# Kernel tuning notes

Hardware: AMD Instinct MI355X
Metric: run time of the kernel (lower is better)

The kernel has to match this reference:

```python
import jax, jax.numpy as jnp
import numpy as np


def setup_inputs() -> dict:
    key = jax.random.key(0)
    k = jax.random.split(key, 6)
    BS, T, ZCH, H, W = 16, 8, 256, 16, 16
    VOCAB, EMB = 4096, 256
    x = jax.random.uniform(k[0], (BS, T, ZCH, H, W), dtype=jnp.float32)
    # Embedding init mirrors uniform_(-1/vocab, 1/vocab)
    codebook = jax.random.uniform(k[1], (VOCAB, EMB), dtype=jnp.float32,
                                  minval=-1.0 / VOCAB, maxval=1.0 / VOCAB)
    pre_w = jax.random.normal(k[2], (EMB, ZCH), dtype=jnp.float32) * 0.02
    pre_b = jax.random.normal(k[3], (EMB,), dtype=jnp.float32) * 0.02
    post_w = jax.random.normal(k[4], (ZCH, EMB), dtype=jnp.float32) * 0.02
    post_b = jax.random.normal(k[5], (ZCH,), dtype=jnp.float32) * 0.02
    return {"x": x, "codebook": codebook, "pre_w": pre_w, "pre_b": pre_b,
            "post_w": post_w, "post_b": post_b}


def reference(x, codebook, pre_w, pre_b, post_w, post_b):
    bs, t, zch, h, w = x.shape
    vocab, emb = codebook.shape
    # preprocess: [0,1] -> [-1,1]
    xp = x * 2.0 - 1.0
    # flatten time into batch; encoder is identity (external module)
    z_in = xp.reshape(bs * t, zch, h, w)
    # pre_quantize_conv: 1x1 conv == per-pixel linear (z_ch -> emb)
    z = jnp.einsum('bchw,ec->behw', z_in, pre_w) + pre_b[None, :, None, None]
    # flatten: (b h w) e  -- matches rearrange('b e h w -> (b h w) e')
    zf = z.transpose(0, 2, 3, 1).reshape(-1, emb)  # [N, emb]
    # squared cdist via expansion: ||z||^2 + ||c||^2 - 2 z.c
    z_sq = jnp.sum(zf * zf, axis=-1, keepdims=True)          # [N,1]
    c_sq = jnp.sum(codebook * codebook, axis=-1)             # [V]
    dist = z_sq + c_sq[None, :] - 2.0 * (zf @ codebook.T)    # [N,V]
    tokens = jnp.argmin(dist, axis=-1)                        # [N]
    zq = codebook[tokens]                                     # [N, emb] gather
    zq = zq.reshape(bs * t, h, w, emb).transpose(0, 3, 1, 2)  # b e h w
    # straight-through estimator
    dec_in = z + jax.lax.stop_gradient(zq - z)
    # post_quantize_conv: 1x1 conv (emb -> z_ch); decoder is identity
    recon = jnp.einsum('behw,ce->bchw', dec_in, post_w) + post_b[None, :, None, None]
    z_out = z.reshape(bs, t, emb, h, w)
    zq_out = zq.reshape(bs, t, emb, h, w)
    recon_out = recon.reshape(bs, t, zch, h, w)
    tokens_out = tokens.reshape(bs, t, h * w)
    return z_out, zq_out, recon_out, tokens_out
```

## Files before the change

kernel.cpp:

```cpp
#include <hip/hip_runtime.h>
#include <float.h>
#include <stdint.h>

#define BB   128
#define CCH  256
#define EMB_ 256
#define HW   256
#define NPIX 32768
#define VOC  4096

typedef _Float16 f16x8 __attribute__((ext_vector_type(8)));
typedef float    f32x4 __attribute__((ext_vector_type(4)));

__device__ __forceinline__ void async16(void* lds, const void* g) {
    __builtin_amdgcn_global_load_lds((const __attribute__((address_space(1))) uint32_t*)g,
                                     (__attribute__((address_space(3))) uint32_t*)lds,
                                     16, 0, 0);
}

__global__ __launch_bounds__(256) void k_prep(const float* __restrict__ cb,
                                              const float* __restrict__ post_w,
                                              const float* __restrict__ post_b,
                                              const float* __restrict__ pre_w,
                                              float* __restrict__ postcode,
                                              _Float16* __restrict__ B3,
                                              float* __restrict__ csq,
                                              _Float16* __restrict__ W3) {
    __shared__ float smem[4352];
    const int bid = blockIdx.x;
    const int tid = threadIdx.x;

    if (bid < 256) {
        float (*cbs)[EMB_] = (float(*)[EMB_])smem;
        int v0 = bid * 16;
        int c  = tid;
#pragma unroll
        for (int r = 0; r < 16; ++r)
            cbs[r][c] = cb[(v0 + r) * EMB_ + c];
        __syncthreads();
        float acc[16];
        float bias = post_b[c];
#pragma unroll
        for (int r = 0; r < 16; ++r) acc[r] = bias;
        const float4* w4p = (const float4*)(post_w + c * EMB_);
        for (int e4 = 0; e4 < 64; ++e4) {
            float4 w4 = w4p[e4];
#pragma unroll
            for (int r = 0; r < 16; ++r) {
                float4 c4 = *(const float4*)&cbs[r][e4 * 4];
                acc[r] = fmaf(w4.x, c4.x, fmaf(w4.y, c4.y,
                         fmaf(w4.z, c4.z, fmaf(w4.w, c4.w, acc[r]))));
            }
        }
#pragma unroll
        for (int r = 0; r < 16; ++r)
            postcode[(v0 + r) * CCH + c] = acc[r];
    } else if (bid < 512) {
        float (*cs)[17] = (float(*)[17])smem;
        int vg = bid - 256;
        int vr = tid >> 4, e0 = (tid & 15) << 4;
        const float* cp = cb + (vg * 16 + vr) * EMB_ + e0;
#pragma unroll
        for (int j = 0; j < 16; ++j)
            cs[e0 + j][vr] = cp[j];
        __syncthreads();
#pragma unroll
        for (int it = 0; it < 4; ++it) {
            int c = it * 256 + tid;
            int kc8 = c >> 4, row = c & 15;
            int lo = kc8 >> 5;
            int kh = kc8 & 31;
            f16x8 outv;
#pragma unroll
            for (int j = 0; j < 8; ++j) {
                float v = cs[kh * 8 + j][row] * 65536.0f;
                _Float16 h = (_Float16)v;
                if (lo) h = (_Float16)(v - (float)h);
                outv[j] = h;
            }
            *(f16x8*)(B3 + ((vg * 64 + kc8) * 128 + row * 8)) = outv;
        }
    } else if (bid < 528) {
        int v = (bid - 512) * 256 + tid;
        const float4* row = (const float4*)(cb + v * EMB_);
        float s = 0.f;
#pragma unroll 8
        for (int q = 0; q < 64; ++q) {
            float4 a = row[q];
            s = fmaf(a.x, a.x, fmaf(a.y, a.y, fmaf(a.z, a.z, fmaf(a.w, a.w, s))));
        }
        csq[v] = s;
    } else {
        int eg = bid - 528;
#pragma unroll
        for (int i = 0; i < 4; ++i) {
            int flat = i * 256 + tid;
            int u = flat >> 4, row = flat & 15;
            int part = u >> 5, c8 = u & 31;
            const float* wp = pre_w + (eg * 16 + row) * CCH + c8 * 8;
            f16x8 outv;
#pragma unroll
            for (int j = 0; j < 8; ++j) {
                float v = wp[j] * 16.0f;
                _Float16 h = (_Float16)v;
                if (part) h = (_Float16)((v - (float)h) * 4096.0f);
                outv[j] = h;
            }
            *(f16x8*)(W3 + ((eg * 64 + u) * 128 + row * 8)) = outv;
        }
    }
}

__global__ __launch_bounds__(512) void k_zgemm(const float* __restrict__ x,
                                               const _Float16* __restrict__ W3,
                                               const float* __restrict__ pre_b,
                                               float* __restrict__ zout,
                                               _Float16* __restrict__ A3) {
    __shared__ __align__(16) char smem[99328];
    float* pbs = (float*)(smem + 98304);

    const int tid = threadIdx.x;
    const int l   = tid & 63;
    const int w   = tid >> 6;
    const int l15 = l & 15, l4 = l >> 4;
    const int wr  = w >> 2, wc = w & 3;
    const int bM  = blockIdx.x;
    const int b   = bM >> 1, hw0 = (bM & 1) * 128;

    const int xng = tid >> 6, xu = (tid >> 4) & 3, xrow = tid & 15;
    const float* xbase = x + (size_t)b * (CCH * HW) + hw0 + xng * 16 + xrow;

#define STAGE_W(CC, BUF) {                                                   \
    _Pragma("unroll")                                                        \
    for (int i = 0; i < 2; ++i) {                                            \
        int flat = i * 512 + tid; int eg = flat >> 6, sub = flat & 63;       \
        async16((_Float16*)(smem + (BUF) * 16384) + flat * 8,                \
                W3 + (eg * 64 + (CC) * 4) * 128 + sub * 8);                  \
        async16((_Float16*)(smem + 32768 + (BUF) * 16384) + flat * 8,        \
                W3 + (eg * 64 + 32 + (CC) * 4) * 128 + sub * 8);             \
    } }

#define STAGE_X(CC, BUF) {                                                   \
    const float* xp_ = xbase + ((CC) * 32 + xu * 8) * HW;                    \
    f16x8 hv, lv;                                                            \
    _Pragma("unroll")                                                        \
    for (int j = 0; j < 8; ++j) {                                            \
        float xv = 2.0f * xp_[j * HW] - 1.0f;                     \
        _Float16 h = (_Float16)xv;                                           \
        lv[j] = (_Float16)((xv - (float)h) * 4096.0f);   \
        hv[j] = h;                                                           \
    }                                                                        \
    *(f16x8*)((_Float16*)(smem + 65536 + (BUF) * 8192) + tid * 8) = hv;      \
    *(f16x8*)((_Float16*)(smem + 81920 + (BUF) * 8192) + tid * 8) = lv;      \
    }

    if (tid < 256) pbs[tid] = pre_b[tid];
    STAGE_W(0, 0)
    STAGE_X(0, 0)
    __syncthreads();

    f32x4 accA[4][4], accB[4][4];
    const f32x4 zero4 = {0.f, 0.f, 0.f, 0.f};
#pragma unroll
    for (int m = 0; m < 4; ++m)
#pragma unroll
        for (int s = 0; s < 4; ++s) { accA[m][s] = zero4; accB[m][s] = zero4; }

    int buf = 0;
    for (int cc = 0; cc < 8; ++cc) {
        if (cc < 7) { STAGE_W(cc + 1, buf ^ 1) STAGE_X(cc + 1, buf ^ 1) }
        const _Float16* WhC = (const _Float16*)(smem + buf * 16384);
        const _Float16* WlC = (const _Float16*)(smem + 32768 + buf * 16384);
        const _Float16* XhC = (const _Float16*)(smem + 65536 + buf * 8192);
        const _Float16* XlC = (const _Float16*)(smem + 81920 + buf * 8192);
        f16x8 whf[4], wlf[4], xhf[4], xlf[4];
#pragma unroll
        for (int m = 0; m < 4; ++m) {
            whf[m] = *(const f16x8*)&WhC[((wc * 4 + m) * 64 + l4 * 16 + l15) * 8];
            wlf[m] = *(const f16x8*)&WlC[((wc * 4 + m) * 64 + l4 * 16 + l15) * 8];
        }
#pragma unroll
        for (int s = 0; s < 4; ++s) {
            xhf[s] = *(const f16x8*)&XhC[((wr * 4 + s) * 64 + l4 * 16 + l15) * 8];
            xlf[s] = *(const f16x8*)&XlC[((wr * 4 + s) * 64 + l4 * 16 + l15) * 8];
        }
#pragma unroll
        for (int m = 0; m < 4; ++m)
#pragma unroll
            for (int s = 0; s < 4; ++s)
                accA[m][s] = __builtin_amdgcn_mfma_f32_16x16x32_f16(whf[m], xhf[s], accA[m][s], 0, 0, 0);
#pragma unroll
        for (int m = 0; m < 4; ++m)
#pragma unroll
            for (int s = 0; s < 4; ++s)
                accB[m][s] = __builtin_amdgcn_mfma_f32_16x16x32_f16(whf[m], xlf[s], accB[m][s], 0, 0, 0);
#pragma unroll
        for (int m = 0; m < 4; ++m)
#pragma unroll
            for (int s = 0; s < 4; ++s)
                accB[m][s] = __builtin_amdgcn_mfma_f32_16x16x32_f16(wlf[m], xhf[s], accB[m][s], 0, 0, 0);
        __syncthreads();
        buf ^= 1;
    }

    float* zw = (float*)(smem + w * 5120);
    const size_t zbase = (size_t)b * (EMB_ * HW) + hw0;
#pragma unroll
    for (int m = 0; m < 4; ++m) {
        asm volatile("s_waitcnt lgkmcnt(0)" ::: "memory");
        __builtin_amdgcn_sched_barrier(0);
        f32x4 zv[4];
#pragma unroll
        for (int s = 0; s < 4; ++s) {
#pragma unroll
            for (int r = 0; r < 4; ++r) {
                float g = fmaf(accB[m][s][r], 0x1p-12f, accA[m][s][r]) * 0x1p-4f;
                zv[s][r] = g + pbs[wc * 64 + m * 16 + l4 * 4 + r];
            }
            *(f32x4*)(zw + (s * 16 + l15) * 20 + l4 * 4) = zv[s];
#pragma unroll
            for (int r = 0; r < 4; ++r)
                zout[zbase + (size_t)(wc * 64 + m * 16 + l4 * 4 + r) * HW
                     + wr * 64 + s * 16 + l15] = zv[s][r];
        }
        asm volatile("s_waitcnt lgkmcnt(0)" ::: "memory");
        __builtin_amdgcn_sched_barrier(0);
#pragma unroll
        for (int o = 0; o < 4; ++o) {
            int flat = o * 64 + l;
            int part = flat >> 7, rest = flat & 127;
            int pg = rest >> 5, uq = (rest >> 4) & 1, row = rest & 15;
            int nloc = pg * 16 + row;
            float4 va = *(const float4*)(zw + nloc * 20 + uq * 8);
            float4 vb = *(const float4*)(zw + nloc * 20 + uq * 8 + 4);
            float vs[8] = {va.x, va.y, va.z, va.w, vb.x, vb.y, vb.z, vb.w};
            f16x8 outv;
#pragma unroll
            for (int j = 0; j < 8; ++j) {
                float v = vs[j] * 256.0f;
                _Float16 h = (_Float16)v;
                if (part) h = (_Float16)(v - (float)h);
                outv[j] = h;
            }
            *(f16x8*)(A3 + ((size_t)(bM * 8 + wr * 4 + pg) * 64
                            + part * 32 + wc * 8 + m * 2 + uq) * 128 + row * 8) = outv;
        }
    }
#undef STAGE_W
#undef STAGE_X
}

__device__ __forceinline__ void issueA(const _Float16* __restrict__ A3, int bM,
                                       int w, int l, _Float16* dst, int kA) {
#pragma unroll
    for (int i = 0; i < 2; ++i) {
        int pg = 2 * w + i;
        const _Float16* g = A3 + ((bM * 16 + pg) * 64 + kA) * 128 + l * 8;
        async16(dst + pg * 512, g);
    }
}

__device__ __forceinline__ void issueB(const _Float16* __restrict__ B3, int vgbase,
                                       int w, int l, _Float16* dst, int kB) {
#pragma unroll
    for (int i = 0; i < 2; ++i) {
        int vg = 2 * w + i;
        const _Float16* g = B3 + ((vgbase + vg) * 64 + kB) * 128 + l * 8;
        async16(dst + vg * 512, g);
    }
}

__global__ __launch_bounds__(512) void k_dist(const float* __restrict__ zout,
                                              const _Float16* __restrict__ A3,
                                              const _Float16* __restrict__ B3,
                                              const float* __restrict__ csq,
                                              float* __restrict__ bestw,
                                              int* __restrict__ bidxw) {
    __shared__ __align__(16) _Float16 Ab[3][8192];
    __shared__ __align__(16) _Float16 Bb[3][8192];
    __shared__ float csq_s[2048];
    __shared__ float zsq_s[256];
    __shared__ float red_b[8][128];
    __shared__ int   red_i[8][128];

    const int tid = threadIdx.x;
    const int l   = tid & 63;
    const int w   = tid >> 6;
    const int l15 = l & 15, l4 = l >> 4;
    const int wr  = w >> 2, wc = w & 3;
    const int bM  = blockIdx.x & 127;
    const int nh  = blockIdx.x >> 7;
    const int vgb = nh * 128;

    issueA(A3, bM, w, l, Ab[0], 0);
    issueB(B3, vgb, w, l, Bb[0], 0);
    issueA(A3, bM, w, l, Ab[1], 4);
    issueB(B3, vgb, w, l, Bb[1], 4);

#pragma unroll
    for (int j = 0; j < 4; ++j) csq_s[j * 512 + tid] = csq[nh * 2048 + j * 512 + tid];

    if (tid < 256) {
        const float* zp = zout + bM * (EMB_ * HW) + tid;
        float s = 0.f;
        for (int k = 0; k < 256; ++k) { float zv = zp[k * HW]; s = fmaf(zv, zv, s); }
        zsq_s[tid] = s;
    }
    __syncthreads();

    float best[32]; int bidx[32];
#pragma unroll
    for (int i = 0; i < 32; ++i) { best[i] = FLT_MAX; bidx[i] = 0; }

    const f32x4 zero4 = {0.f, 0.f, 0.f, 0.f};
    int cur = 0;
    for (int vt = 0; vt < 8; ++vt) {
        f32x4 acc[8][4];
#pragma unroll
        for (int s = 0; s < 8; ++s)
#pragma unroll
            for (int m = 0; m < 4; ++m) acc[s][m] = zero4;

        for (int kc = 0; kc < 24; ++kc) {
            const int n = vt * 24 + kc;
            int kc2 = kc + 2, vt2 = vt;
            if (kc2 >= 24) { kc2 -= 24; ++vt2; }
            const int nxt = (cur + 2 >= 3) ? cur - 1 : cur + 2;
            const bool pf = (vt2 < 8);
            const int kA2 = ((kc2 >= 16) ? 32 : 0) + (kc2 & 7) * 4;
            const int kB2 = ((kc2 >= 8 && kc2 < 16) ? 32 : 0) + (kc2 & 7) * 4;

            f16x8 af0[4], bf[4];
#pragma unroll
            for (int s = 0; s < 4; ++s)
                af0[s] = *(const f16x8*)&Ab[cur][(wr * 8 + s) * 512 + l4 * 128 + l15 * 8];
#pragma unroll
            for (int m = 0; m < 4; ++m)
                bf[m] = *(const f16x8*)&Bb[cur][(wc * 4 + m) * 512 + l4 * 128 + l15 * 8];
            if (pf) issueA(A3, bM, w, l, Ab[nxt], kA2);
            __builtin_amdgcn_s_barrier();
            asm volatile("s_waitcnt lgkmcnt(0)" ::: "memory");
            __builtin_amdgcn_sched_barrier(0);
            __builtin_amdgcn_s_setprio(1);
#pragma unroll
            for (int s = 0; s < 4; ++s)
#pragma unroll
                for (int m = 0; m < 4; ++m)
                    acc[s][m] = __builtin_amdgcn_mfma_f32_16x16x32_f16(af0[s], bf[m], acc[s][m], 0, 0, 0);
            __builtin_amdgcn_s_setprio(0);
            __builtin_amdgcn_s_barrier();

            f16x8 af1[4];
#pragma unroll
            for (int s = 0; s < 4; ++s)
                af1[s] = *(const f16x8*)&Ab[cur][(wr * 8 + 4 + s) * 512 + l4 * 128 + l15 * 8];
            if (pf) issueB(B3, vgb + vt2 * 16, w, l, Bb[nxt], kB2);
            __builtin_amdgcn_s_barrier();
            asm volatile("s_waitcnt lgkmcnt(0)" ::: "memory");
            __builtin_amdgcn_sched_barrier(0);
            __builtin_amdgcn_s_setprio(1);
#pragma unroll
            for (int s = 0; s < 4; ++s)
#pragma unroll
                for (int m = 0; m < 4; ++m)
                    acc[4 + s][m] = __builtin_amdgcn_mfma_f32_16x16x32_f16(af1[s], bf[m], acc[4 + s][m], 0, 0, 0);
            __builtin_amdgcn_s_setprio(0);
            if (n == 190) { asm volatile("s_waitcnt vmcnt(0)" ::: "memory"); }
            else          { asm volatile("s_waitcnt vmcnt(4)" ::: "memory"); }
            __builtin_amdgcn_s_barrier();
            __builtin_amdgcn_sched_barrier(0);
            cur = (cur + 1 >= 3) ? 0 : cur + 1;
        }

#pragma unroll
        for (int m = 0; m < 4; ++m) {
            int cl = vt * 256 + (wc * 4 + m) * 16 + l15;
            float cs = csq_s[cl];
            int code = nh * 2048 + cl;
#pragma unroll
            for (int s = 0; s < 8; ++s)
#pragma unroll
                for (int r = 0; r < 4; ++r) {
                    float dd = (zsq_s[wr * 128 + s * 16 + l4 * 4 + r] + cs)
                               - acc[s][m][r] * 0x1p-23f;
                    int pi = s * 4 + r;
                    if (dd < best[pi]) { best[pi] = dd; bidx[pi] = code; }
                }
        }
    }

#pragma unroll
    for (int off = 8; off >= 1; off >>= 1) {
#pragma unroll
        for (int i = 0; i < 32; ++i) {
            float ob = __shfl_xor(best[i], off, 64);
            int   oi = __shfl_xor(bidx[i], off, 64);
            if (ob < best[i] || (ob == best[i] && oi < bidx[i])) { best[i] = ob; bidx[i] = oi; }
        }
    }
    if (l15 == 0) {
#pragma unroll
        for (int s = 0; s < 8; ++s)
#pragma unroll
            for (int r = 0; r < 4; ++r) {
                int pl = s * 16 + l4 * 4 + r;
                red_b[w][pl] = best[s * 4 + r];
                red_i[w][pl] = bidx[s * 4 + r];
            }
    }
    __syncthreads();
    if (tid < 256) {
        int wrg = tid >> 7, pl = tid & 127;
        float bb = red_b[wrg * 4][pl]; int bi = red_i[wrg * 4][pl];
#pragma unroll
        for (int c = 1; c < 4; ++c) {
            float ob = red_b[wrg * 4 + c][pl]; int oi = red_i[wrg * 4 + c][pl];
            if (ob < bb || (ob == bb && oi < bi)) { bb = ob; bi = oi; }
        }
        bestw[nh * NPIX + bM * 256 + tid] = bb;
        bidxw[nh * NPIX + bM * 256 + tid] = bi;
    }
}

__global__ __launch_bounds__(256) void k_argmin2(const float* __restrict__ bestw,
                                                 const int* __restrict__ bidxw,
                                                 float* __restrict__ tok_f) {
    int i = blockIdx.x * 256 + threadIdx.x;
    float b0 = bestw[i], b1 = bestw[NPIX + i];
    int   i0 = bidxw[i], i1 = bidxw[NPIX + i];
    tok_f[i] = (float)((b1 < b0) ? i1 : i0);
}

__global__ __launch_bounds__(256) void k_gather(const float* __restrict__ tok_f,
                                                const float* __restrict__ cb,
                                                const float* __restrict__ postcode,
                                                float* __restrict__ zq_out,
                                                float* __restrict__ recon) {
    int b  = blockIdx.x >> 3;
    int e0 = (blockIdx.x & 7) * 32;
    int hw = threadIdx.x;
    int t  = (int)tok_f[b * HW + hw];
    const float* cbr = cb       + t * EMB_;
    const float* pcr = postcode + t * CCH;
    float* zq = zq_out + b * (EMB_ * HW) + hw;
    float* rc = recon  + b * (CCH * HW) + hw;
#pragma unroll
    for (int j = 0; j < 32; ++j) {
        int e = e0 + j;
        zq[e * HW] = cbr[e];
        rc[e * HW] = pcr[e];
    }
}

__global__ __launch_bounds__(256) void k_gather_fused(const float* __restrict__ bestw,
                                                      const int* __restrict__ bidxw,
                                                      const float* __restrict__ cb,
                                                      const float* __restrict__ postcode,
                                                      float* __restrict__ zq_out,
                                                      float* __restrict__ recon,
                                                      float* __restrict__ tok_f) {
    int b  = blockIdx.x >> 3;
    int e0 = (blockIdx.x & 7) * 32;
    int hw = threadIdx.x;
    int i  = b * HW + hw;
    float b0 = bestw[i], b1 = bestw[NPIX + i];
    int   i0 = bidxw[i], i1 = bidxw[NPIX + i];
    int   t  = (b1 < b0) ? i1 : i0;
    if (e0 == 0) tok_f[i] = (float)t;
    const float* cbr = cb       + t * EMB_;
    const float* pcr = postcode + t * CCH;
    float* zq = zq_out + b * (EMB_ * HW) + hw;
    float* rc = recon  + b * (CCH * HW) + hw;
#pragma unroll
    for (int j = 0; j < 32; ++j) {
        int e = e0 + j;
        zq[e * HW] = cbr[e];
        rc[e * HW] = pcr[e];
    }
}

extern "C" void kernel_launch(void* const* d_in, const int* in_sizes, int n_in,
                              void* d_out, int out_size, void* d_ws, size_t ws_size,
                              hipStream_t stream) {
    const float* x      = (const float*)d_in[0];
    const float* cb     = (const float*)d_in[1];
    const float* pre_w  = (const float*)d_in[2];
    const float* pre_b  = (const float*)d_in[3];
    const float* post_w = (const float*)d_in[4];
    const float* post_b = (const float*)d_in[5];

    float* out    = (float*)d_out;
    float* z_out  = out;
    float* zq_out = out + 8388608;
    float* recon  = out + 16777216;
    float* tok_f  = out + 25165824;

    _Float16* A3 = (_Float16*)zq_out;
    _Float16* B3 = (_Float16*)recon;
    _Float16* W3 = (_Float16*)(recon + 1048576 + 4 * NPIX);

    float* csq      = (float*)d_ws;
    float* postcode = csq + VOC;

    size_t need = (size_t)(VOC + VOC * CCH + 4 * NPIX) * sizeof(float);
    bool fused = (ws_size >= need);
    float* bestw; int* bidxw;
    if (fused) {
        bestw = postcode + (size_t)VOC * CCH;
        bidxw = (int*)(bestw + 2 * NPIX);
    } else {
        bestw = recon + 1048576;
        bidxw = (int*)(recon + 1048576 + 2 * NPIX);
    }

    k_prep <<< 544, 256, 0, stream>>>(cb, post_w, post_b, pre_w,
                                      postcode, B3, csq, W3);
    k_zgemm<<< 256, 512, 0, stream>>>(x, W3, pre_b, z_out, A3);
    k_dist <<< 256, 512, 0, stream>>>(z_out, A3, B3, csq, bestw, bidxw);
    if (fused) {
        k_gather_fused<<<1024, 256, 0, stream>>>(bestw, bidxw, cb, postcode,
                                                 zq_out, recon, tok_f);
    } else {
        k_argmin2<<< 128, 256, 0, stream>>>(bestw, bidxw, tok_f);
        k_gather <<<1024, 256, 0, stream>>>(tok_f, cb, postcode, zq_out, recon);
    }
}
```

Before: 391.3 us.

## Deepen distance-kernel prefetch to four stages and stage gather rows through LDS

The distance GEMM kernel moves from three to four LDS buffers and prefetches three K-chunks ahead, with the vmcnt waits adjusted so more async global-to-LDS loads stay in flight. The gather kernel is rewritten so each block reads whole codebook and postcode rows coalesced into a padded LDS tile, then writes the transposed output coalesced by pixel. Both target memory latency and uncoalesced access, at the cost of more LDS per block, which may lower occupancy in the distance kernel, and fewer, larger gather blocks (256 instead of 1024).

```diff
diff --git a/kernel.cpp b/kernel.cpp
--- a/kernel.cpp
+++ b/kernel.cpp
@@ -276,8 +276,8 @@
                                               const float* __restrict__ csq,
                                               float* __restrict__ bestw,
                                               int* __restrict__ bidxw) {
-    __shared__ __align__(16) _Float16 Ab[3][8192];
-    __shared__ __align__(16) _Float16 Bb[3][8192];
+    __shared__ __align__(16) _Float16 Ab[4][8192];
+    __shared__ __align__(16) _Float16 Bb[4][8192];
     __shared__ float csq_s[2048];
     __shared__ float zsq_s[256];
     __shared__ float red_b[8][128];
@@ -292,10 +292,9 @@
     const int nh  = blockIdx.x >> 7;
     const int vgb = nh * 128;
 
-    issueA(A3, bM, w, l, Ab[0], 0);
-    issueB(B3, vgb, w, l, Bb[0], 0);
-    issueA(A3, bM, w, l, Ab[1], 4);
-    issueB(B3, vgb, w, l, Bb[1], 4);
+    issueA(A3, bM, w, l, Ab[0], 0);  issueB(B3, vgb, w, l, Bb[0], 0);
+    issueA(A3, bM, w, l, Ab[1], 4);  issueB(B3, vgb, w, l, Bb[1], 4);
+    issueA(A3, bM, w, l, Ab[2], 8);  issueB(B3, vgb, w, l, Bb[2], 8);
 
 #pragma unroll
     for (int j = 0; j < 4; ++j) csq_s[j * 512 + tid] = csq[nh * 2048 + j * 512 + tid];
@@ -323,12 +322,12 @@
 
         for (int kc = 0; kc < 24; ++kc) {
             const int n = vt * 24 + kc;
-            int kc2 = kc + 2, vt2 = vt;
-            if (kc2 >= 24) { kc2 -= 24; ++vt2; }
-            const int nxt = (cur + 2 >= 3) ? cur - 1 : cur + 2;
-            const bool pf = (vt2 < 8);
-            const int kA2 = ((kc2 >= 16) ? 32 : 0) + (kc2 & 7) * 4;
-            const int kB2 = ((kc2 >= 8 && kc2 < 16) ? 32 : 0) + (kc2 & 7) * 4;
+            int kc3 = kc + 3, vt3 = vt;
+            if (kc3 >= 24) { kc3 -= 24; ++vt3; }
+            const int nxt = (cur + 3) & 3;
+            const bool pf = (vt3 < 8);
+            const int kA3 = ((kc3 >= 16) ? 32 : 0) + (kc3 & 7) * 4;
+            const int kB3 = ((kc3 >= 8 && kc3 < 16) ? 32 : 0) + (kc3 & 7) * 4;
 
             f16x8 af0[4], bf[4];
 #pragma unroll
@@ -337,7 +336,7 @@
 #pragma unroll
             for (int m = 0; m < 4; ++m)
                 bf[m] = *(const f16x8*)&Bb[cur][(wc * 4 + m) * 512 + l4 * 128 + l15 * 8];
-            if (pf) issueA(A3, bM, w, l, Ab[nxt], kA2);
+            if (pf) issueA(A3, bM, w, l, Ab[nxt], kA3);
             __builtin_amdgcn_s_barrier();
             asm volatile("s_waitcnt lgkmcnt(0)" ::: "memory");
             __builtin_amdgcn_sched_barrier(0);
@@ -354,7 +353,7 @@
 #pragma unroll
             for (int s = 0; s < 4; ++s)
                 af1[s] = *(const f16x8*)&Ab[cur][(wr * 8 + 4 + s) * 512 + l4 * 128 + l15 * 8];
-            if (pf) issueB(B3, vgb + vt2 * 16, w, l, Bb[nxt], kB2);
+            if (pf) issueB(B3, vgb + vt3 * 16, w, l, Bb[nxt], kB3);
             __builtin_amdgcn_s_barrier();
             asm volatile("s_waitcnt lgkmcnt(0)" ::: "memory");
             __builtin_amdgcn_sched_barrier(0);
@@ -365,11 +364,12 @@
                 for (int m = 0; m < 4; ++m)
                     acc[4 + s][m] = __builtin_amdgcn_mfma_f32_16x16x32_f16(af1[s], bf[m], acc[4 + s][m], 0, 0, 0);
             __builtin_amdgcn_s_setprio(0);
-            if (n == 190) { asm volatile("s_waitcnt vmcnt(0)" ::: "memory"); }
-            else          { asm volatile("s_waitcnt vmcnt(4)" ::: "memory"); }
+            if (n <= 188)      { asm volatile("s_waitcnt vmcnt(8)" ::: "memory"); }
+            else if (n == 189) { asm volatile("s_waitcnt vmcnt(4)" ::: "memory"); }
+            else               { asm volatile("s_waitcnt vmcnt(0)" ::: "memory"); }
             __builtin_amdgcn_s_barrier();
             __builtin_amdgcn_sched_barrier(0);
-            cur = (cur + 1 >= 3) ? 0 : cur + 1;
+            cur = (cur + 1) & 3;
         }
 
 #pragma unroll
@@ -452,30 +452,57 @@
     }
 }
 
-__global__ __launch_bounds__(256) void k_gather_fused(const float* __restrict__ bestw,
-                                                      const int* __restrict__ bidxw,
-                                                      const float* __restrict__ cb,
-                                                      const float* __restrict__ postcode,
-                                                      float* __restrict__ zq_out,
-                                                      float* __restrict__ recon,
-                                                      float* __restrict__ tok_f) {
-    int b  = blockIdx.x >> 3;
-    int e0 = (blockIdx.x & 7) * 32;
-    int hw = threadIdx.x;
-    int i  = b * HW + hw;
-    float b0 = bestw[i], b1 = bestw[NPIX + i];
-    int   i0 = bidxw[i], i1 = bidxw[NPIX + i];
-    int   t  = (b1 < b0) ? i1 : i0;
-    if (e0 == 0) tok_f[i] = (float)t;
-    const float* cbr = cb       + t * EMB_;
-    const float* pcr = postcode + t * CCH;
-    float* zq = zq_out + b * (EMB_ * HW) + hw;
-    float* rc = recon  + b * (CCH * HW) + hw;
-#pragma unroll
-    for (int j = 0; j < 32; ++j) {
-        int e = e0 + j;
-        zq[e * HW] = cbr[e];
-        rc[e * HW] = pcr[e];
+__global__ __launch_bounds__(256) void k_gather2(const float* __restrict__ bestw,
+                                                 const int* __restrict__ bidxw,
+                                                 const float* __restrict__ cb,
+                                                 const float* __restrict__ postcode,
+                                                 float* __restrict__ zq_out,
+                                                 float* __restrict__ recon,
+                                                 float* __restrict__ tok_f) {
+    __shared__ float rows[64][257];
+    __shared__ int   toks[64];
+    const int b    = blockIdx.x >> 1;
+    const int half = blockIdx.x & 1;
+    const int tid  = threadIdx.x;
+    const int p    = tid & 63, eg = tid >> 6;
+
+    for (int g = 0; g < 2; ++g) {
+        int px0 = half * 128 + g * 64;
+        if (tid < 64) {
+            int i = b * HW + px0 + tid;
+            float b0 = bestw[i], b1 = bestw[NPIX + i];
+            int   i0 = bidxw[i], i1 = bidxw[NPIX + i];
+            int t = (b1 < b0) ? i1 : i0;
+            toks[tid] = t;
+            tok_f[i] = (float)t;
+        }
+        __syncthreads();
+#pragma unroll 8
+        for (int r = 0; r < 64; ++r)
+            rows[r][tid] = cb[(size_t)toks[r] * EMB_ + tid];
+        __syncthreads();
+        {
+            float* zq = zq_out + (size_t)b * (EMB_ * HW) + px0 + p;
+#pragma unroll 8
+            for (int eo = 0; eo < 64; ++eo) {
+                int e = eg * 64 + eo;
+                zq[(size_t)e * HW] = rows[p][e];
+            }
+        }
+        __syncthreads();
+#pragma unroll 8
+        for (int r = 0; r < 64; ++r)
+            rows[r][tid] = postcode[(size_t)toks[r] * CCH + tid];
+        __syncthreads();
+        {
+            float* rc = recon + (size_t)b * (CCH * HW) + px0 + p;
+#pragma unroll 8
+            for (int eo = 0; eo < 64; ++eo) {
+                int e = eg * 64 + eo;
+                rc[(size_t)e * HW] = rows[p][e];
+            }
+        }
+        __syncthreads();
     }
 }
 
@@ -518,8 +545,8 @@
     k_zgemm<<< 256, 512, 0, stream>>>(x, W3, pre_b, z_out, A3);
     k_dist <<< 256, 512, 0, stream>>>(z_out, A3, B3, csq, bestw, bidxw);
     if (fused) {
-        k_gather_fused<<<1024, 256, 0, stream>>>(bestw, bidxw, cb, postcode,
-                                                 zq_out, recon, tok_f);
+        k_gather2<<< 256, 256, 0, stream>>>(bestw, bidxw, cb, postcode,
+                                            zq_out, recon, tok_f);
     } else {
         k_argmin2<<< 128, 256, 0, stream>>>(bestw, bidxw, tok_f);
         k_gather <<<1024, 256, 0, stream>>>(tok_f, cb, postcode, zq_out, recon);
```

Result: no change. 390.6 us (-0.2%).
